# Kernel tuning notes

Hardware: AMD Instinct MI355X
Metric: run time of the kernel (lower is better)

## Reference

```python
import jax, jax.numpy as jnp
import numpy as np

IN, H, B = 256, 256, 65536


def setup_inputs() -> dict:
    key = jax.random.key(0)
    ks = jax.random.split(key, 20)
    s_in = 1.0 / np.sqrt(IN)
    s_h = 1.0 / np.sqrt(H)
    d = {
        "input": jax.random.normal(ks[0], (B, IN), jnp.float32),
        "hidden": jax.random.normal(ks[1], (B, H), jnp.float32),
        "cell": jax.random.normal(ks[2], (B, H), jnp.float32),
    }
    names_i = ["Wif", "Wii", "Wio", "Wig"]
    names_h = ["Whf", "Whi", "Who", "Whg"]
    for j, n in enumerate(names_i):
        d[n] = jax.random.uniform(ks[3 + j], (H, IN), jnp.float32, -s_in, s_in)
        d["b" + n[1:]] = jax.random.uniform(ks[7 + j], (H,), jnp.float32, -s_in, s_in)
    for j, n in enumerate(names_h):
        d[n] = jax.random.uniform(ks[11 + j], (H, H), jnp.float32, -s_h, s_h)
        d["b" + n[1:]] = jax.random.uniform(ks[15 + j], (H,), jnp.float32, -s_h, s_h)
    return d


def reference(input, hidden, cell,
              Wif, bif, Wii, bii, Wio, bio, Wig, big,
              Whf, bhf, Whi, bhi, Who, bho, Whg, bhg):
    # Fuse the 8 small linears into two [*,4H] GEMMs (same math as 8 separate Linear calls)
    Wi = jnp.concatenate([Wif, Wii, Wio, Wig], axis=0)  # [4H, IN]
    Wh = jnp.concatenate([Whf, Whi, Who, Whg], axis=0)  # [4H, H]
    bi = jnp.concatenate([bif, bii, bio, big])
    bh = jnp.concatenate([bhf, bhi, bho, bhg])
    gates = input @ Wi.T + bi + hidden @ Wh.T + bh  # [B, 4H]
    f, i, o, g = jnp.split(gates, 4, axis=1)
    f = jax.nn.sigmoid(f)
    i = jax.nn.sigmoid(i)
    o = jax.nn.sigmoid(o)
    g = jnp.tanh(g)
    new_cell = f * cell + i * g
    new_hidden = o * jnp.tanh(new_cell)
    output = jax.nn.log_softmax(new_hidden, axis=1)
    return output, new_hidden, new_cell
```

## Files before the change

kernel.cpp:

```cpp
#include <hip/hip_runtime.h>
#include <hip/hip_bf16.h>
#include <stdint.h>


#define BH 16777216

typedef float f32x4 __attribute__((ext_vector_type(4)));
typedef short short8 __attribute__((ext_vector_type(8)));

__device__ __forceinline__ unsigned short f2bf(float f) {
    union { float f; unsigned u; } v; v.f = f;
    unsigned u = v.u;
    return (unsigned short)((u + 0x7fffu + ((u >> 16) & 1u)) >> 16);
}

__device__ __forceinline__ unsigned pack2bf(float a, float b) {
    __hip_bfloat162 h = __float22bfloat162_rn(make_float2(a, b));
    union { __hip_bfloat162 h; unsigned u; } v; v.h = h;
    return v.u;
}

__device__ __forceinline__ float sigm(float x) { return 1.f / (1.f + __expf(-x)); }
__device__ __forceinline__ float tanh_(float x) { return 1.f - 2.f / (1.f + __expf(2.f * x)); }

__device__ __forceinline__ void glds16(const unsigned short* g, const unsigned short* l) {
    __builtin_amdgcn_global_load_lds(
        (const __attribute__((address_space(1))) unsigned int*)(uintptr_t)g,
        (__attribute__((address_space(3))) unsigned int*)(unsigned int)(uintptr_t)l,
        16, 0, 0);
}

__global__ __launch_bounds__(256) void pack_kernel(
    const float* __restrict__ Wif, const float* __restrict__ Wii,
    const float* __restrict__ Wio, const float* __restrict__ Wig,
    const float* __restrict__ Whf, const float* __restrict__ Whi,
    const float* __restrict__ Who, const float* __restrict__ Whg,
    const float* __restrict__ bif, const float* __restrict__ bii,
    const float* __restrict__ bio, const float* __restrict__ big,
    const float* __restrict__ bhf, const float* __restrict__ bhi,
    const float* __restrict__ bho, const float* __restrict__ bhg,
    unsigned short* __restrict__ wpack, float* __restrict__ bpack)
{
    const int t = blockIdx.x * 256 + threadIdx.x;
    const int n16  = t & 15;
    const int kg   = (t >> 4) & 3;
    const int Nt   = (t >> 6) & 15;
    const int step = (t >> 10) & 15;
    const int hg   = t >> 14;
    const int gate = Nt & 3;
    const int wc   = Nt >> 2;
    const int h    = hg * 64 + wc * 16 + n16;
    const int k0   = step * 32 + kg * 8;

    const float* Wi = (gate == 0) ? Wif : (gate == 1) ? Wii : (gate == 2) ? Wio : Wig;
    const float* Wh = (gate == 0) ? Whf : (gate == 1) ? Whi : (gate == 2) ? Who : Whg;
    const float* src = (k0 < 256) ? (Wi + h * 256 + k0) : (Wh + h * 256 + (k0 - 256));

    unsigned pk[4];
#pragma unroll
    for (int p = 0; p < 4; ++p)
        pk[p] = (unsigned)f2bf(src[p * 2]) | ((unsigned)f2bf(src[p * 2 + 1]) << 16);
    uint4 o4 = {pk[0], pk[1], pk[2], pk[3]};
    *(uint4*)&wpack[(size_t)t * 8] = o4;

    if (t < 1024) {
        const int cp = t;
        const int n2 = cp & 15, Nt2 = (cp >> 4) & 15, hg2 = cp >> 8;
        const int g2 = Nt2 & 3, wc2 = Nt2 >> 2;
        const int h2 = hg2 * 64 + wc2 * 16 + n2;
        const float* bi = (g2 == 0) ? bif : (g2 == 1) ? bii : (g2 == 2) ? bio : big;
        const float* bh = (g2 == 0) ? bhf : (g2 == 1) ? bhi : (g2 == 2) ? bho : bhg;
        bpack[cp] = bi[h2] + bh[h2];
    }
}

__global__ __launch_bounds__(512, 4) void lstm_gemm_kernel(
    const float* __restrict__ input, const float* __restrict__ hidden,
    const float* __restrict__ cell,
    const unsigned short* __restrict__ wpack, const float* __restrict__ bpack,
    float* __restrict__ out)
{
    __shared__ unsigned short buf[2][12288];

    const int swz = (blockIdx.x & 7) * 256 + (blockIdx.x >> 3);
    const int hg  = swz & 3;
    const int row0 = (swz >> 2) * 128;

    const int tid = threadIdx.x;
    const int w = tid >> 6, l = tid & 63;
    const int wr = w >> 2, wc = w & 3;
    const int srow = tid >> 2;
    const int skc  = tid & 3;

    const unsigned short* wsrc = wpack + (((size_t)hg * 16) << 13) + w * 1024 + l * 8;

    {
        glds16(wsrc, &buf[0][4096 + w * 1024]);
        glds16(wsrc + 512, &buf[0][4096 + w * 1024 + 512]);
        const float* asrc = input + (size_t)(row0 + srow) * 256 + skc * 8;
        float4 x0 = *(const float4*)asrc;
        float4 x1 = *(const float4*)(asrc + 4);
        uint4 o; o.x = pack2bf(x0.x, x0.y); o.y = pack2bf(x0.z, x0.w);
        o.z = pack2bf(x1.x, x1.y); o.w = pack2bf(x1.z, x1.w);
        *(uint4*)&buf[0][((srow >> 4) * 64 + skc * 16 + (srow & 15)) << 3] = o;
    }
    __syncthreads();

    f32x4 acc[4][4] = {};

#pragma unroll 2
    for (int step = 0; step < 16; ++step) {
        const int cb = step & 1, nb = cb ^ 1;
        float4 x0, x1;
        if (step < 15) {
            const unsigned short* ws = wsrc + ((size_t)(step + 1) << 13);
            glds16(ws, &buf[nb][4096 + w * 1024]);
            glds16(ws + 512, &buf[nb][4096 + w * 1024 + 512]);
            const int k0 = (step + 1) * 32 + skc * 8;
            const float* asrc = (k0 < 256)
                ? input  + (size_t)(row0 + srow) * 256 + k0
                : hidden + (size_t)(row0 + srow) * 256 + (k0 - 256);
            x0 = *(const float4*)asrc;
            x1 = *(const float4*)(asrc + 4);
        }
        short8 Af[4], Bf[4];
#pragma unroll
        for (int m = 0; m < 4; ++m)
            Af[m] = *(const short8*)&buf[cb][((wr * 4 + m) * 64 + l) << 3];
#pragma unroll
        for (int n = 0; n < 4; ++n)
            Bf[n] = *(const short8*)&buf[cb][4096 + (((wc * 4 + n) * 64 + l) << 3)];
#pragma unroll
        for (int m = 0; m < 4; ++m)
#pragma unroll
            for (int n = 0; n < 4; ++n)
                acc[m][n] = __builtin_amdgcn_mfma_f32_16x16x32_bf16(Af[m], Bf[n], acc[m][n], 0, 0, 0);
        if (step < 15) {
            uint4 o; o.x = pack2bf(x0.x, x0.y); o.y = pack2bf(x0.z, x0.w);
            o.z = pack2bf(x1.x, x1.y); o.w = pack2bf(x1.z, x1.w);
            *(uint4*)&buf[nb][((srow >> 4) * 64 + skc * 16 + (srow & 15)) << 3] = o;
        }
        __syncthreads();
    }

    const int n16 = l & 15;
    const int lrow = l >> 4;
    const int hcol = hg * 64 + wc * 16 + n16;
    float bias[4];
#pragma unroll
    for (int n = 0; n < 4; ++n)
        bias[n] = bpack[hg * 256 + wc * 64 + n * 16 + n16];

#pragma unroll
    for (int m = 0; m < 4; ++m) {
#pragma unroll
        for (int rr = 0; rr < 4; ++rr) {
            const size_t rg_ = (size_t)row0 + wr * 64 + m * 16 + lrow * 4 + rr;
            const float fv = sigm(acc[m][0][rr] + bias[0]);
            const float iv = sigm(acc[m][1][rr] + bias[1]);
            const float ov = sigm(acc[m][2][rr] + bias[2]);
            const float gv = tanh_(acc[m][3][rr] + bias[3]);
            const float cv = cell[rg_ * 256 + hcol];
            const float nc = fv * cv + iv * gv;
            const float nhv = ov * tanh_(nc);
            out[(size_t)2 * BH + rg_ * 256 + hcol] = nc;
            out[(size_t)BH + rg_ * 256 + hcol] = nhv;
        }
    }
}

__global__ __launch_bounds__(256) void softmax_kernel(
    const float* __restrict__ nh, float* __restrict__ outp)
{
    const int w = threadIdx.x >> 6, l = threadIdx.x & 63;
#pragma unroll 1
    for (int it = 0; it < 8; ++it) {
        const size_t row = (size_t)it * 8192 + blockIdx.x * 4 + w;
        float4 v = *(const float4*)(nh + row * 256 + l * 4);
        float s = __expf(v.x) + __expf(v.y) + __expf(v.z) + __expf(v.w);
#pragma unroll
        for (int m = 1; m < 64; m <<= 1) s += __shfl_xor(s, m);
        const float lz = __logf(s);
        float4 o = {v.x - lz, v.y - lz, v.z - lz, v.w - lz};
        *(float4*)(outp + row * 256 + l * 4) = o;
    }
}

extern "C" void kernel_launch(void* const* d_in, const int* in_sizes, int n_in,
                              void* d_out, int out_size, void* d_ws, size_t ws_size,
                              hipStream_t stream)
{
    const float* input  = (const float*)d_in[0];
    const float* hidden = (const float*)d_in[1];
    const float* cell   = (const float*)d_in[2];
    const float* Wif = (const float*)d_in[3];  const float* bif = (const float*)d_in[4];
    const float* Wii = (const float*)d_in[5];  const float* bii = (const float*)d_in[6];
    const float* Wio = (const float*)d_in[7];  const float* bio = (const float*)d_in[8];
    const float* Wig = (const float*)d_in[9];  const float* big = (const float*)d_in[10];
    const float* Whf = (const float*)d_in[11]; const float* bhf = (const float*)d_in[12];
    const float* Whi = (const float*)d_in[13]; const float* bhi = (const float*)d_in[14];
    const float* Who = (const float*)d_in[15]; const float* bho = (const float*)d_in[16];
    const float* Whg = (const float*)d_in[17]; const float* bhg = (const float*)d_in[18];

    unsigned short* wpack = (unsigned short*)d_ws;
    float* bpack = (float*)((char*)d_ws + (size_t)1024 * 512 * 2);

    hipLaunchKernelGGL(pack_kernel, dim3(256), dim3(256), 0, stream,
        Wif, Wii, Wio, Wig, Whf, Whi, Who, Whg,
        bif, bii, bio, big, bhf, bhi, bho, bhg, wpack, bpack);

    float* out = (float*)d_out;
    hipLaunchKernelGGL(lstm_gemm_kernel, dim3(2048), dim3(512), 0, stream,
        input, hidden, cell, wpack, bpack, out);

    hipLaunchKernelGGL(softmax_kernel, dim3(2048), dim3(256), 0, stream,
        out + (size_t)BH, out);
}
```

Before: 168.0 us.

## Pre-convert activations to packed bf16 and load via direct-to-LDS copies

Adds a separate kernel that converts input and hidden from fp32 to bf16 in the MFMA tile layout, writing into the output buffer as scratch. The GEMM kernel then streams A tiles with direct global-to-LDS loads, as it already does for weights, instead of doing register loads, conversion and LDS stores inside the main loop. This takes conversion work and register pressure out of the GEMM's critical path. In exchange it adds an extra pass that reads 128 MB of fp32 and writes 64 MB of bf16, and it reuses the output buffer as scratch, which is only safe if the GEMM never overwrites packed data that other blocks still need to read.

```diff
diff --git a/kernel.cpp b/kernel.cpp
--- a/kernel.cpp
+++ b/kernel.cpp
@@ -74,8 +74,28 @@
     }
 }
 
+__global__ __launch_bounds__(256) void convert_kernel(
+    const float* __restrict__ input, const float* __restrict__ hidden,
+    unsigned short* __restrict__ xpack)
+{
+    const int t = blockIdx.x * 256 + threadIdx.x;
+    const int l     = t & 63;
+    const int rt    = (t >> 6) & 7;
+    const int step  = (t >> 9) & 15;
+    const int panel = t >> 13;
+    const int row = panel * 128 + rt * 16 + (l & 15);
+    const int k0  = step * 32 + (l >> 4) * 8;
+    const float* src = (k0 < 256) ? input + (size_t)row * 256 + k0
+                                  : hidden + (size_t)row * 256 + (k0 - 256);
+    float4 x0 = *(const float4*)src;
+    float4 x1 = *(const float4*)(src + 4);
+    uint4 o; o.x = pack2bf(x0.x, x0.y); o.y = pack2bf(x0.z, x0.w);
+    o.z = pack2bf(x1.x, x1.y); o.w = pack2bf(x1.z, x1.w);
+    *(uint4*)&xpack[(size_t)t * 8] = o;
+}
+
 __global__ __launch_bounds__(512, 4) void lstm_gemm_kernel(
-    const float* __restrict__ input, const float* __restrict__ hidden,
+    const unsigned short* __restrict__ xpack,
     const float* __restrict__ cell,
     const unsigned short* __restrict__ wpack, const float* __restrict__ bpack,
     float* __restrict__ out)
@@ -83,27 +103,20 @@
     __shared__ unsigned short buf[2][12288];
 
     const int swz = (blockIdx.x & 7) * 256 + (blockIdx.x >> 3);
-    const int hg  = swz & 3;
-    const int row0 = (swz >> 2) * 128;
+    const int hg    = swz & 3;
+    const int panel = swz >> 2;
+    const int row0  = panel * 128;
 
     const int tid = threadIdx.x;
     const int w = tid >> 6, l = tid & 63;
     const int wr = w >> 2, wc = w & 3;
-    const int srow = tid >> 2;
-    const int skc  = tid & 3;
-
-    const unsigned short* wsrc = wpack + (((size_t)hg * 16) << 13) + w * 1024 + l * 8;
-
-    {
-        glds16(wsrc, &buf[0][4096 + w * 1024]);
-        glds16(wsrc + 512, &buf[0][4096 + w * 1024 + 512]);
-        const float* asrc = input + (size_t)(row0 + srow) * 256 + skc * 8;
-        float4 x0 = *(const float4*)asrc;
-        float4 x1 = *(const float4*)(asrc + 4);
-        uint4 o; o.x = pack2bf(x0.x, x0.y); o.y = pack2bf(x0.z, x0.w);
-        o.z = pack2bf(x1.x, x1.y); o.w = pack2bf(x1.z, x1.w);
-        *(uint4*)&buf[0][((srow >> 4) * 64 + skc * 16 + (srow & 15)) << 3] = o;
-    }
+
+    const unsigned short* asrc = xpack + (size_t)panel * 65536 + w * 512 + l * 8;
+    const unsigned short* wsrc = wpack + (size_t)hg * 131072 + w * 1024 + l * 8;
+
+    glds16(asrc, &buf[0][w * 512]);
+    glds16(wsrc, &buf[0][4096 + w * 1024]);
+    glds16(wsrc + 512, &buf[0][4096 + w * 1024 + 512]);
     __syncthreads();
 
     f32x4 acc[4][4] = {};
@@ -111,17 +124,10 @@
 #pragma unroll 2
     for (int step = 0; step < 16; ++step) {
         const int cb = step & 1, nb = cb ^ 1;
-        float4 x0, x1;
         if (step < 15) {
-            const unsigned short* ws = wsrc + ((size_t)(step + 1) << 13);
-            glds16(ws, &buf[nb][4096 + w * 1024]);
-            glds16(ws + 512, &buf[nb][4096 + w * 1024 + 512]);
-            const int k0 = (step + 1) * 32 + skc * 8;
-            const float* asrc = (k0 < 256)
-                ? input  + (size_t)(row0 + srow) * 256 + k0
-                : hidden + (size_t)(row0 + srow) * 256 + (k0 - 256);
-            x0 = *(const float4*)asrc;
-            x1 = *(const float4*)(asrc + 4);
+            glds16(asrc + (size_t)(step + 1) * 4096, &buf[nb][w * 512]);
+            glds16(wsrc + (size_t)(step + 1) * 8192, &buf[nb][4096 + w * 1024]);
+            glds16(wsrc + (size_t)(step + 1) * 8192 + 512, &buf[nb][4096 + w * 1024 + 512]);
         }
         short8 Af[4], Bf[4];
 #pragma unroll
@@ -135,11 +141,6 @@
 #pragma unroll
             for (int n = 0; n < 4; ++n)
                 acc[m][n] = __builtin_amdgcn_mfma_f32_16x16x32_bf16(Af[m], Bf[n], acc[m][n], 0, 0, 0);
-        if (step < 15) {
-            uint4 o; o.x = pack2bf(x0.x, x0.y); o.y = pack2bf(x0.z, x0.w);
-            o.z = pack2bf(x1.x, x1.y); o.w = pack2bf(x1.z, x1.w);
-            *(uint4*)&buf[nb][((srow >> 4) * 64 + skc * 16 + (srow & 15)) << 3] = o;
-        }
         __syncthreads();
     }
 
@@ -205,13 +206,18 @@
     unsigned short* wpack = (unsigned short*)d_ws;
     float* bpack = (float*)((char*)d_ws + (size_t)1024 * 512 * 2);
 
+    float* out = (float*)d_out;
+    unsigned short* xpack = (unsigned short*)d_out;
+
     hipLaunchKernelGGL(pack_kernel, dim3(256), dim3(256), 0, stream,
         Wif, Wii, Wio, Wig, Whf, Whi, Who, Whg,
         bif, bii, bio, big, bhf, bhi, bho, bhg, wpack, bpack);
 
-    float* out = (float*)d_out;
+    hipLaunchKernelGGL(convert_kernel, dim3(16384), dim3(256), 0, stream,
+        input, hidden, xpack);
+
     hipLaunchKernelGGL(lstm_gemm_kernel, dim3(2048), dim3(512), 0, stream,
-        input, hidden, cell, wpack, bpack, out);
+        xpack, cell, wpack, bpack, out);
 
     hipLaunchKernelGGL(softmax_kernel, dim3(2048), dim3(256), 0, stream,
         out + (size_t)BH, out);
```

Result: slower. 179.1 us (+6.6%).
